# Performance work log

Hardware: AMD Instinct MI355X
Metric: run time of the kernel (lower is better)

The kernel has to match this reference:

```python
import jax, jax.numpy as jnp
import numpy as np

C = 1024      # BIGNET_DIM
GROUPS = 256  # (1024*1024) / group_size(4096)

def _dequant(q4, norm):
    # q4: [GROUPS, 2048] ints in [0,256) packing two 4-bit codes per byte
    # (even positions = low nibble, odd positions = high nibble, as in
    #  block_quantize_4bit / block_dequantize_4bit). norm: [GROUPS, 1].
    lo = q4 % 16
    hi = q4 // 16
    q8 = jnp.stack([lo, hi], axis=-1).reshape(GROUPS, -1).astype(jnp.float32)  # [GROUPS, 4096]
    w = (q8 / 15.0 * 2.0 - 1.0) * norm
    return w.reshape(C, C)  # [out_features, in_features]

def setup_inputs() -> dict:
    key = jax.random.key(0)
    ks = jax.random.split(key, 6)
    x = jax.random.normal(ks[0], (16384, C), jnp.float32)
    wq4 = jax.random.randint(ks[1], (18, GROUPS, 2048), 0, 256, jnp.int32)
    wnorm = jax.random.uniform(ks[2], (18, GROUPS, 1), dtype=jnp.float32) * 0.05 + 1e-3
    lora_a = jax.random.normal(ks[3], (3, 32, C), jnp.float32) * 0.02
    lora_b = jax.random.normal(ks[4], (3, C, 32), jnp.float32) * 0.01
    ln_gamma = jnp.ones((5, C), jnp.float32)
    ln_beta = jnp.zeros((5, C), jnp.float32)
    return {"x": x, "wq4": wq4, "wnorm": wnorm, "lora_a": lora_a,
            "lora_b": lora_b, "ln_gamma": ln_gamma, "ln_beta": ln_beta}

def reference(x, wq4, wnorm, lora_a, lora_b, ln_gamma, ln_beta):
    def lin(h, i):
        # dequantize group-wise int4 weight, then linear (bias=False)
        return h @ _dequant(wq4[i], wnorm[i]).T

    def block(h, b, li):
        y = lin(h, 3 * b)
        if li is not None:  # QLoRALinear: parallel fp32 low-rank path
            y = y + (h @ lora_a[li].T) @ lora_b[li].T
        y = jax.nn.relu(y)
        y = jax.nn.relu(lin(y, 3 * b + 1))
        y = lin(y, 3 * b + 2)
        return y + h  # residual

    def ln(h, i):
        mu = jnp.mean(h, axis=-1, keepdims=True)
        var = jnp.mean((h - mu) ** 2, axis=-1, keepdims=True)
        return (h - mu) * jax.lax.rsqrt(var + 1e-5) * ln_gamma[i] + ln_beta[i]

    h = block(x, 0, 0); h = ln(h, 0)
    h = block(h, 1, None); h = ln(h, 1)
    h = block(h, 2, 1); h = ln(h, 2)
    h = block(h, 3, None); h = ln(h, 3)
    h = block(h, 4, 2); h = ln(h, 4)
    h = block(h, 5, None)
    return h
```

## Files before the change

kernel.cpp:

```cpp
#include <hip/hip_runtime.h>

typedef __bf16 bf16x8 __attribute__((ext_vector_type(8)));
typedef float f32x4 __attribute__((ext_vector_type(4)));

__device__ __forceinline__ unsigned short f32_to_bf16u(float f) {
  unsigned int u = __float_as_uint(f);
  u += 0x7fffu + ((u >> 16) & 1u);
  return (unsigned short)(u >> 16);
}

__device__ __forceinline__ void async_copy16(const void* gptr, void* lptr) {
  __builtin_amdgcn_global_load_lds(
      (__attribute__((address_space(1))) void*)(unsigned long long)gptr,
      (__attribute__((address_space(3))) void*)(unsigned long long)lptr,
      16, 0, 0);
}

__global__ __launch_bounds__(256) void dequant_kernel(
    const int* __restrict__ wq4, const float* __restrict__ wnorm,
    const float* __restrict__ lora_a, const float* __restrict__ lora_b,
    unsigned short* __restrict__ Wd)
{
  const int gi = blockIdx.x * 256 + threadIdx.x;
  const int w = gi >> 19;
  const int rem = gi & 524287;
  const int q = wq4[gi];
  const float norm = wnorm[(w << 8) + (rem >> 11)];
  float w0 = (float)(q & 15) * (2.0f / 15.0f) - 1.0f;
  float w1 = (float)(q >> 4) * (2.0f / 15.0f) - 1.0f;
  w0 *= norm;
  w1 *= norm;
  const int p = rem << 1;
  const int li = (w == 0) ? 0 : (w == 6) ? 1 : (w == 12) ? 2 : -1;
  if (li >= 0) {
    const int o = p >> 10;
    const int col = p & 1023;
    const float* Ar = lora_a + li * 32768 + col;
    const float* Br = lora_b + li * 32768 + o * 32;
    float s0 = 0.f, s1 = 0.f;
#pragma unroll
    for (int r = 0; r < 32; r++) {
      const float br = Br[r];
      s0 += br * Ar[r * 1024];
      s1 += br * Ar[r * 1024 + 1];
    }
    w0 += s0;
    w1 += s1;
  }
  const unsigned int packed =
      ((unsigned int)f32_to_bf16u(w1) << 16) | (unsigned int)f32_to_bf16u(w0);
  *(unsigned int*)&Wd[((size_t)w << 20) + p] = packed;
}

__global__ __launch_bounds__(256) void cast_bf16_kernel(
    const float* __restrict__ x, unsigned short* __restrict__ o)
{
  const int i = blockIdx.x * 256 + threadIdx.x;
  const float4 v = ((const float4*)x)[i];
  ushort4 b;
  b.x = f32_to_bf16u(v.x);
  b.y = f32_to_bf16u(v.y);
  b.z = f32_to_bf16u(v.z);
  b.w = f32_to_bf16u(v.w);
  ((ushort4*)o)[i] = b;
}

template <int EPIL>
__global__ __launch_bounds__(256, 4) void gemm_bt(
    const unsigned short* __restrict__ A, const unsigned short* __restrict__ W,
    void* __restrict__ Out, const float* __restrict__ Res)
{
  constexpr int K = 1024;
  constexpr int N = 1024;
  __shared__ unsigned short As[128 * 64];
  __shared__ unsigned short Ws[128 * 64];

  const int tid = threadIdx.x;
  const int lane = tid & 63;
  const int wave = tid >> 6;

  const int bid = blockIdx.x;
  const int xcd = bid & 7;
  const int j = bid >> 3;
  const int m0 = (xcd * 16 + (j >> 3)) * 128;
  const int n0 = (j & 7) * 128;

  const int wm = (wave >> 1) * 64;
  const int wn = (wave & 1) * 64;

  f32x4 acc[4][4];
#pragma unroll
  for (int i = 0; i < 4; i++)
#pragma unroll
    for (int jj = 0; jj < 4; jj++) acc[i][jj] = (f32x4){0.f, 0.f, 0.f, 0.f};

  const int arow = tid >> 3;
  const int acol8 = (tid & 7) ^ (arow & 7);
  const unsigned short* Ag = A + (size_t)(m0 + arow) * K + acol8 * 8;
  const unsigned short* Wg = W + (size_t)(n0 + arow) * K + acol8 * 8;
  unsigned short* Asd = &As[tid * 8];
  unsigned short* Wsd = &Ws[tid * 8];

  const int fr = lane & 15;
  const int q = lane >> 4;

  for (int k0 = 0; k0 < K; k0 += 64) {
#pragma unroll
    for (int i = 0; i < 4; i++)
      async_copy16(Ag + (size_t)i * 32 * K + k0, Asd + i * 2048);
#pragma unroll
    for (int i = 0; i < 4; i++)
      async_copy16(Wg + (size_t)i * 32 * K + k0, Wsd + i * 2048);
    __syncthreads();
#pragma unroll
    for (int h = 0; h < 2; h++) {
      const int kk8 = q + h * 4;
      bf16x8 a[4], b[4];
#pragma unroll
      for (int i = 0; i < 4; i++) {
        const int row = wm + i * 16 + fr;
        a[i] = *(const bf16x8*)&As[row * 64 + ((kk8 ^ (fr & 7)) << 3)];
      }
#pragma unroll
      for (int jj = 0; jj < 4; jj++) {
        const int row = wn + jj * 16 + fr;
        b[jj] = *(const bf16x8*)&Ws[row * 64 + ((kk8 ^ (fr & 7)) << 3)];
      }
#pragma unroll
      for (int i = 0; i < 4; i++)
#pragma unroll
        for (int jj = 0; jj < 4; jj++)
          acc[i][jj] = __builtin_amdgcn_mfma_f32_16x16x32_bf16(a[i], b[jj], acc[i][jj], 0, 0, 0);
    }
    __syncthreads();
  }

  const int rq = q * 4;
#pragma unroll
  for (int i = 0; i < 4; i++) {
#pragma unroll
    for (int r = 0; r < 4; r++) {
      const int m = m0 + wm + i * 16 + rq + r;
#pragma unroll
      for (int jj = 0; jj < 4; jj++) {
        const int n = n0 + wn + jj * 16 + fr;
        float v = acc[i][jj][r];
        if (EPIL == 0) {
          v = v > 0.f ? v : 0.f;
          ((unsigned short*)Out)[(size_t)m * N + n] = f32_to_bf16u(v);
        } else {
          ((float*)Out)[(size_t)m * N + n] = v + Res[(size_t)m * N + n];
        }
      }
    }
  }
}

__global__ __launch_bounds__(256) void ln_kernel(
    const float* __restrict__ y, const float* __restrict__ gamma,
    const float* __restrict__ beta, unsigned short* __restrict__ h_bf,
    float* __restrict__ h_f32)
{
  const int row = blockIdx.x;
  const int tid = threadIdx.x;
  const size_t base = (size_t)row * 1024;
  const float4 v = ((const float4*)(y + base))[tid];
  float s = v.x + v.y + v.z + v.w;
  float s2 = v.x * v.x + v.y * v.y + v.z * v.z + v.w * v.w;
#pragma unroll
  for (int off = 32; off > 0; off >>= 1) {
    s += __shfl_down(s, off, 64);
    s2 += __shfl_down(s2, off, 64);
  }
  __shared__ float red[8];
  if ((tid & 63) == 0) {
    red[tid >> 6] = s;
    red[4 + (tid >> 6)] = s2;
  }
  __syncthreads();
  s = red[0] + red[1] + red[2] + red[3];
  s2 = red[4] + red[5] + red[6] + red[7];
  const float mu = s * (1.0f / 1024.0f);
  const float var = s2 * (1.0f / 1024.0f) - mu * mu;
  const float rs = rsqrtf(var + 1e-5f);
  const float4 g = ((const float4*)gamma)[tid];
  const float4 bb = ((const float4*)beta)[tid];
  float4 o;
  o.x = (v.x - mu) * rs * g.x + bb.x;
  o.y = (v.y - mu) * rs * g.y + bb.y;
  o.z = (v.z - mu) * rs * g.z + bb.z;
  o.w = (v.w - mu) * rs * g.w + bb.w;
  ((float4*)(h_f32 + base))[tid] = o;
  ushort4 ob;
  ob.x = f32_to_bf16u(o.x);
  ob.y = f32_to_bf16u(o.y);
  ob.z = f32_to_bf16u(o.z);
  ob.w = f32_to_bf16u(o.w);
  ((ushort4*)(h_bf + base))[tid] = ob;
}

extern "C" void kernel_launch(void* const* d_in, const int* in_sizes, int n_in,
                              void* d_out, int out_size, void* d_ws, size_t ws_size,
                              hipStream_t stream)
{
  const float* x = (const float*)d_in[0];
  const int* wq4 = (const int*)d_in[1];
  const float* wnorm = (const float*)d_in[2];
  const float* lora_a = (const float*)d_in[3];
  const float* lora_b = (const float*)d_in[4];
  const float* ln_g = (const float*)d_in[5];
  const float* ln_b = (const float*)d_in[6];
  float* out = (float*)d_out;

  char* ws = (char*)d_ws;
  unsigned short* Wd   = (unsigned short*)(ws);
  unsigned short* h_bf = (unsigned short*)(ws + 37748736);
  unsigned short* t1   = (unsigned short*)(ws + 71303168);
  unsigned short* t2   = (unsigned short*)(ws + 104857600);
  float* h_f32         = (float*)(ws + 138412032);

  dequant_kernel<<<36864, 256, 0, stream>>>(wq4, wnorm, lora_a, lora_b, Wd);
  cast_bf16_kernel<<<16384, 256, 0, stream>>>(x, h_bf);

  const unsigned short* hb = h_bf;
  const float* hres = x;
  for (int b = 0; b < 6; b++) {
    const unsigned short* W0 = Wd + (size_t)(3 * b + 0) * 1048576;
    const unsigned short* W1 = Wd + (size_t)(3 * b + 1) * 1048576;
    const unsigned short* W2 = Wd + (size_t)(3 * b + 2) * 1048576;
    gemm_bt<0><<<1024, 256, 0, stream>>>(hb, W0, t1, nullptr);
    gemm_bt<0><<<1024, 256, 0, stream>>>(t1, W1, t2, nullptr);
    gemm_bt<1><<<1024, 256, 0, stream>>>(t2, W2, out, hres);
    if (b < 5) {
      ln_kernel<<<16384, 256, 0, stream>>>(out, ln_g + b * 1024, ln_b + b * 1024,
                                           h_bf, h_f32);
      hb = h_bf;
      hres = h_f32;
    }
  }
  (void)in_sizes; (void)n_in; (void)out_size; (void)ws_size;
}
```

Measured before the change: 1.041 ms.

## Stage GEMM epilogue through LDS for coalesced stores; precompute LoRA B·A

The GEMM epilogue now writes accumulators into shared memory and then issues 16-byte coalesced global stores. The residual-add variant also reads Res with float4 loads, in two half-tile passes so it fits in 32 KB of LDS. This replaces scattered 2- and 4-byte stores. Separately, the LoRA B·A product is computed once in its own kernel into scratch, reusing the h_f32 buffer before it is needed. Dequant then just adds that product instead of doing a 32-term dot product per element. The cost is extra barriers and LDS traffic in the epilogue.

```diff
diff --git a/kernel.cpp b/kernel.cpp
--- a/kernel.cpp
+++ b/kernel.cpp
@@ -2,6 +2,7 @@
 
 typedef __bf16 bf16x8 __attribute__((ext_vector_type(8)));
 typedef float f32x4 __attribute__((ext_vector_type(4)));
+typedef unsigned short ushort8 __attribute__((ext_vector_type(8)));
 
 __device__ __forceinline__ unsigned short f32_to_bf16u(float f) {
   unsigned int u = __float_as_uint(f);
@@ -16,36 +17,43 @@
       16, 0, 0);
 }
 
+__global__ __launch_bounds__(256) void lora_ba_kernel(
+    const float* __restrict__ lora_a, const float* __restrict__ lora_b,
+    float* __restrict__ Wba)
+{
+  const int bid = blockIdx.x;
+  const int li = bid >> 10;
+  const int o = bid & 1023;
+  const float* B = lora_b + li * 32768 + o * 32;
+  const float* A = lora_a + li * 32768;
+  const int c = threadIdx.x * 4;
+  float4 acc = {0.f, 0.f, 0.f, 0.f};
+#pragma unroll
+  for (int r = 0; r < 32; r++) {
+    const float br = B[r];
+    const float4 a = *(const float4*)&A[r * 1024 + c];
+    acc.x += br * a.x; acc.y += br * a.y; acc.z += br * a.z; acc.w += br * a.w;
+  }
+  *(float4*)&Wba[((size_t)li << 20) + o * 1024 + c] = acc;
+}
+
 __global__ __launch_bounds__(256) void dequant_kernel(
     const int* __restrict__ wq4, const float* __restrict__ wnorm,
-    const float* __restrict__ lora_a, const float* __restrict__ lora_b,
-    unsigned short* __restrict__ Wd)
+    const float* __restrict__ Wba, unsigned short* __restrict__ Wd)
 {
   const int gi = blockIdx.x * 256 + threadIdx.x;
   const int w = gi >> 19;
   const int rem = gi & 524287;
   const int q = wq4[gi];
   const float norm = wnorm[(w << 8) + (rem >> 11)];
-  float w0 = (float)(q & 15) * (2.0f / 15.0f) - 1.0f;
-  float w1 = (float)(q >> 4) * (2.0f / 15.0f) - 1.0f;
-  w0 *= norm;
-  w1 *= norm;
+  float w0 = ((float)(q & 15) * (2.0f / 15.0f) - 1.0f) * norm;
+  float w1 = ((float)(q >> 4) * (2.0f / 15.0f) - 1.0f) * norm;
   const int p = rem << 1;
   const int li = (w == 0) ? 0 : (w == 6) ? 1 : (w == 12) ? 2 : -1;
   if (li >= 0) {
-    const int o = p >> 10;
-    const int col = p & 1023;
-    const float* Ar = lora_a + li * 32768 + col;
-    const float* Br = lora_b + li * 32768 + o * 32;
-    float s0 = 0.f, s1 = 0.f;
-#pragma unroll
-    for (int r = 0; r < 32; r++) {
-      const float br = Br[r];
-      s0 += br * Ar[r * 1024];
-      s1 += br * Ar[r * 1024 + 1];
-    }
-    w0 += s0;
-    w1 += s1;
+    const float2 ba = *(const float2*)&Wba[((size_t)li << 20) + p];
+    w0 += ba.x;
+    w1 += ba.y;
   }
   const unsigned int packed =
       ((unsigned int)f32_to_bf16u(w1) << 16) | (unsigned int)f32_to_bf16u(w0);
@@ -72,8 +80,9 @@
 {
   constexpr int K = 1024;
   constexpr int N = 1024;
-  __shared__ unsigned short As[128 * 64];
-  __shared__ unsigned short Ws[128 * 64];
+  __shared__ __align__(16) char smem[32768];
+  unsigned short* As = (unsigned short*)smem;
+  unsigned short* Ws = (unsigned short*)(smem + 16384);
 
   const int tid = threadIdx.x;
   const int lane = tid & 63;
@@ -136,22 +145,59 @@
   }
 
   const int rq = q * 4;
-#pragma unroll
-  for (int i = 0; i < 4; i++) {
-#pragma unroll
-    for (int r = 0; r < 4; r++) {
-      const int m = m0 + wm + i * 16 + rq + r;
-#pragma unroll
-      for (int jj = 0; jj < 4; jj++) {
-        const int n = n0 + wn + jj * 16 + fr;
-        float v = acc[i][jj][r];
-        if (EPIL == 0) {
+
+  if (EPIL == 0) {
+    unsigned short* cs = (unsigned short*)smem;
+#pragma unroll
+    for (int i = 0; i < 4; i++)
+#pragma unroll
+      for (int r = 0; r < 4; r++) {
+        const int m = wm + i * 16 + rq + r;
+#pragma unroll
+        for (int jj = 0; jj < 4; jj++) {
+          const int n = wn + jj * 16 + fr;
+          float v = acc[i][jj][r];
           v = v > 0.f ? v : 0.f;
-          ((unsigned short*)Out)[(size_t)m * N + n] = f32_to_bf16u(v);
-        } else {
-          ((float*)Out)[(size_t)m * N + n] = v + Res[(size_t)m * N + n];
+          cs[m * 128 + n] = f32_to_bf16u(v);
         }
       }
+    __syncthreads();
+#pragma unroll
+    for (int it = 0; it < 8; it++) {
+      const int flat16 = it * 256 + tid;
+      const int row = flat16 >> 4;
+      const int unit = flat16 & 15;
+      const ushort8 v = *(const ushort8*)&cs[flat16 * 8];
+      *(ushort8*)&((unsigned short*)Out)[(size_t)(m0 + row) * N + n0 + unit * 8] = v;
+    }
+  } else {
+    float* cf = (float*)smem;
+#pragma unroll
+    for (int half = 0; half < 2; half++) {
+      if ((wave >> 1) == half) {
+#pragma unroll
+        for (int i = 0; i < 4; i++)
+#pragma unroll
+          for (int r = 0; r < 4; r++) {
+            const int mrel = i * 16 + rq + r;
+#pragma unroll
+            for (int jj = 0; jj < 4; jj++)
+              cf[mrel * 128 + wn + jj * 16 + fr] = acc[i][jj][r];
+          }
+      }
+      __syncthreads();
+#pragma unroll
+      for (int it = 0; it < 8; it++) {
+        const int flat4 = it * 256 + tid;
+        const int row = flat4 >> 5;
+        const int unit = flat4 & 31;
+        const size_t g = (size_t)(m0 + half * 64 + row) * N + n0 + unit * 4;
+        float4 v = *(const float4*)&cf[flat4 * 4];
+        const float4 rr = *(const float4*)&Res[g];
+        v.x += rr.x; v.y += rr.y; v.z += rr.z; v.w += rr.w;
+        *(float4*)&((float*)Out)[g] = v;
+      }
+      __syncthreads();
     }
   }
 }
@@ -218,8 +264,10 @@
   unsigned short* t1   = (unsigned short*)(ws + 71303168);
   unsigned short* t2   = (unsigned short*)(ws + 104857600);
   float* h_f32         = (float*)(ws + 138412032);
-
-  dequant_kernel<<<36864, 256, 0, stream>>>(wq4, wnorm, lora_a, lora_b, Wd);
+  float* Wba           = (float*)(ws + 138412032);
+
+  lora_ba_kernel<<<3072, 256, 0, stream>>>(lora_a, lora_b, Wba);
+  dequant_kernel<<<36864, 256, 0, stream>>>(wq4, wnorm, Wba, Wd);
   cast_bf16_kernel<<<16384, 256, 0, stream>>>(x, h_bf);
 
   const unsigned short* hb = h_bf;
```

Result: slower. 1.137 ms (+9.3%).

## Keep residual stream in bf16 and precompute LoRA BA product once

Applied to the files above, without the earlier changes.

The residual sum after each block's last GEMM and the LayerNorm output are now stored only in bf16. This drops the fp32 output write, the fp32 residual read and the separate fp32 LayerNorm copy, which roughly halves memory traffic in the epilogues and in the LN kernel. A new kernel computes each LoRA B·A matrix once, so the dequant kernel no longer repeats a 32-term dot product per weight element. The cost is a less accurate residual path, since the residual is rounded to bf16 at every block and may drift from the fp32 reference.

```diff
diff --git a/kernel.cpp b/kernel.cpp
--- a/kernel.cpp
+++ b/kernel.cpp
@@ -7,6 +7,9 @@
   unsigned int u = __float_as_uint(f);
   u += 0x7fffu + ((u >> 16) & 1u);
   return (unsigned short)(u >> 16);
+}
+__device__ __forceinline__ float bf16u_to_f32(unsigned short s) {
+  return __uint_as_float((unsigned int)s << 16);
 }
 
 __device__ __forceinline__ void async_copy16(const void* gptr, void* lptr) {
@@ -16,36 +19,43 @@
       16, 0, 0);
 }
 
+__global__ __launch_bounds__(256) void lora_ba_kernel(
+    const float* __restrict__ lora_a, const float* __restrict__ lora_b,
+    float* __restrict__ Wba)
+{
+  const int bid = blockIdx.x;
+  const int li = bid >> 10;
+  const int o = bid & 1023;
+  const float* B = lora_b + li * 32768 + o * 32;
+  const float* A = lora_a + li * 32768;
+  const int c = threadIdx.x * 4;
+  float4 acc = {0.f, 0.f, 0.f, 0.f};
+#pragma unroll
+  for (int r = 0; r < 32; r++) {
+    const float br = B[r];
+    const float4 a = *(const float4*)&A[r * 1024 + c];
+    acc.x += br * a.x; acc.y += br * a.y; acc.z += br * a.z; acc.w += br * a.w;
+  }
+  *(float4*)&Wba[((size_t)li << 20) + o * 1024 + c] = acc;
+}
+
 __global__ __launch_bounds__(256) void dequant_kernel(
     const int* __restrict__ wq4, const float* __restrict__ wnorm,
-    const float* __restrict__ lora_a, const float* __restrict__ lora_b,
-    unsigned short* __restrict__ Wd)
+    const float* __restrict__ Wba, unsigned short* __restrict__ Wd)
 {
   const int gi = blockIdx.x * 256 + threadIdx.x;
   const int w = gi >> 19;
   const int rem = gi & 524287;
   const int q = wq4[gi];
   const float norm = wnorm[(w << 8) + (rem >> 11)];
-  float w0 = (float)(q & 15) * (2.0f / 15.0f) - 1.0f;
-  float w1 = (float)(q >> 4) * (2.0f / 15.0f) - 1.0f;
-  w0 *= norm;
-  w1 *= norm;
+  float w0 = ((float)(q & 15) * (2.0f / 15.0f) - 1.0f) * norm;
+  float w1 = ((float)(q >> 4) * (2.0f / 15.0f) - 1.0f) * norm;
   const int p = rem << 1;
   const int li = (w == 0) ? 0 : (w == 6) ? 1 : (w == 12) ? 2 : -1;
   if (li >= 0) {
-    const int o = p >> 10;
-    const int col = p & 1023;
-    const float* Ar = lora_a + li * 32768 + col;
-    const float* Br = lora_b + li * 32768 + o * 32;
-    float s0 = 0.f, s1 = 0.f;
-#pragma unroll
-    for (int r = 0; r < 32; r++) {
-      const float br = Br[r];
-      s0 += br * Ar[r * 1024];
-      s1 += br * Ar[r * 1024 + 1];
-    }
-    w0 += s0;
-    w1 += s1;
+    const float2 ba = *(const float2*)&Wba[((size_t)li << 20) + p];
+    w0 += ba.x;
+    w1 += ba.y;
   }
   const unsigned int packed =
       ((unsigned int)f32_to_bf16u(w1) << 16) | (unsigned int)f32_to_bf16u(w0);
@@ -68,7 +78,7 @@
 template <int EPIL>
 __global__ __launch_bounds__(256, 4) void gemm_bt(
     const unsigned short* __restrict__ A, const unsigned short* __restrict__ W,
-    void* __restrict__ Out, const float* __restrict__ Res)
+    void* __restrict__ Out, const unsigned short* __restrict__ Res)
 {
   constexpr int K = 1024;
   constexpr int N = 1024;
@@ -148,8 +158,12 @@
         if (EPIL == 0) {
           v = v > 0.f ? v : 0.f;
           ((unsigned short*)Out)[(size_t)m * N + n] = f32_to_bf16u(v);
+        } else if (EPIL == 1) {
+          v += bf16u_to_f32(Res[(size_t)m * N + n]);
+          ((unsigned short*)Out)[(size_t)m * N + n] = f32_to_bf16u(v);
         } else {
-          ((float*)Out)[(size_t)m * N + n] = v + Res[(size_t)m * N + n];
+          v += bf16u_to_f32(Res[(size_t)m * N + n]);
+          ((float*)Out)[(size_t)m * N + n] = v;
         }
       }
     }
@@ -157,16 +171,17 @@
 }
 
 __global__ __launch_bounds__(256) void ln_kernel(
-    const float* __restrict__ y, const float* __restrict__ gamma,
-    const float* __restrict__ beta, unsigned short* __restrict__ h_bf,
-    float* __restrict__ h_f32)
+    const unsigned short* __restrict__ s_bf, const float* __restrict__ gamma,
+    const float* __restrict__ beta, unsigned short* __restrict__ h_bf)
 {
   const int row = blockIdx.x;
   const int tid = threadIdx.x;
   const size_t base = (size_t)row * 1024;
-  const float4 v = ((const float4*)(y + base))[tid];
-  float s = v.x + v.y + v.z + v.w;
-  float s2 = v.x * v.x + v.y * v.y + v.z * v.z + v.w * v.w;
+  const ushort4 u = ((const ushort4*)(s_bf + base))[tid];
+  float v0 = bf16u_to_f32(u.x), v1 = bf16u_to_f32(u.y);
+  float v2 = bf16u_to_f32(u.z), v3 = bf16u_to_f32(u.w);
+  float s = v0 + v1 + v2 + v3;
+  float s2 = v0 * v0 + v1 * v1 + v2 * v2 + v3 * v3;
 #pragma unroll
   for (int off = 32; off > 0; off >>= 1) {
     s += __shfl_down(s, off, 64);
@@ -185,17 +200,11 @@
   const float rs = rsqrtf(var + 1e-5f);
   const float4 g = ((const float4*)gamma)[tid];
   const float4 bb = ((const float4*)beta)[tid];
-  float4 o;
-  o.x = (v.x - mu) * rs * g.x + bb.x;
-  o.y = (v.y - mu) * rs * g.y + bb.y;
-  o.z = (v.z - mu) * rs * g.z + bb.z;
-  o.w = (v.w - mu) * rs * g.w + bb.w;
-  ((float4*)(h_f32 + base))[tid] = o;
   ushort4 ob;
-  ob.x = f32_to_bf16u(o.x);
-  ob.y = f32_to_bf16u(o.y);
-  ob.z = f32_to_bf16u(o.z);
-  ob.w = f32_to_bf16u(o.w);
+  ob.x = f32_to_bf16u((v0 - mu) * rs * g.x + bb.x);
+  ob.y = f32_to_bf16u((v1 - mu) * rs * g.y + bb.y);
+  ob.z = f32_to_bf16u((v2 - mu) * rs * g.z + bb.z);
+  ob.w = f32_to_bf16u((v3 - mu) * rs * g.w + bb.w);
   ((ushort4*)(h_bf + base))[tid] = ob;
 }
 
@@ -214,28 +223,32 @@
 
   char* ws = (char*)d_ws;
   unsigned short* Wd   = (unsigned short*)(ws);
-  unsigned short* h_bf = (unsigned short*)(ws + 37748736);
+  unsigned short* x_bf = (unsigned short*)(ws + 37748736);
   unsigned short* t1   = (unsigned short*)(ws + 71303168);
   unsigned short* t2   = (unsigned short*)(ws + 104857600);
-  float* h_f32         = (float*)(ws + 138412032);
-
-  dequant_kernel<<<36864, 256, 0, stream>>>(wq4, wnorm, lora_a, lora_b, Wd);
-  cast_bf16_kernel<<<16384, 256, 0, stream>>>(x, h_bf);
-
-  const unsigned short* hb = h_bf;
-  const float* hres = x;
+  unsigned short* s_bf = (unsigned short*)(ws + 138412032);
+  unsigned short* h_bf = (unsigned short*)(ws + 171966464);
+  float* Wba           = (float*)(ws + 138412032);
+
+  lora_ba_kernel<<<3072, 256, 0, stream>>>(lora_a, lora_b, Wba);
+  dequant_kernel<<<36864, 256, 0, stream>>>(wq4, wnorm, Wba, Wd);
+  cast_bf16_kernel<<<16384, 256, 0, stream>>>(x, x_bf);
+
+  const unsigned short* hb = x_bf;
+  const unsigned short* hres = x_bf;
   for (int b = 0; b < 6; b++) {
     const unsigned short* W0 = Wd + (size_t)(3 * b + 0) * 1048576;
     const unsigned short* W1 = Wd + (size_t)(3 * b + 1) * 1048576;
     const unsigned short* W2 = Wd + (size_t)(3 * b + 2) * 1048576;
     gemm_bt<0><<<1024, 256, 0, stream>>>(hb, W0, t1, nullptr);
     gemm_bt<0><<<1024, 256, 0, stream>>>(t1, W1, t2, nullptr);
-    gemm_bt<1><<<1024, 256, 0, stream>>>(t2, W2, out, hres);
     if (b < 5) {
-      ln_kernel<<<16384, 256, 0, stream>>>(out, ln_g + b * 1024, ln_b + b * 1024,
-                                           h_bf, h_f32);
+      gemm_bt<1><<<1024, 256, 0, stream>>>(t2, W2, s_bf, hres);
+      ln_kernel<<<16384, 256, 0, stream>>>(s_bf, ln_g + b * 1024, ln_b + b * 1024, h_bf);
       hb = h_bf;
-      hres = h_f32;
+      hres = h_bf;
+    } else {
+      gemm_bt<2><<<1024, 256, 0, stream>>>(t2, W2, out, hres);
     }
   }
   (void)in_sizes; (void)n_in; (void)out_size; (void)ws_size;
```

Measured after the change: 931.6 us. -10.5%, faster.
